# Optimization experiments

Measured on AMD Instinct MI355X. Metric: run time of the kernel, lower is better.

The kernel has to match this reference:

```python
import jax, jax.numpy as jnp
import numpy as np

B, C, H, W = 32, 128, 32, 32
E, K, D, HID = 16, 2, 128, 512  # nbExperts, topK, nbIn=nbOut, hidden=4*max(nbIn,nbOut)


def setup_inputs() -> dict:
    key = jax.random.key(0)
    ks = jax.random.split(key, 6)
    init = lambda k, shape, fan: (jax.random.normal(k, shape, jnp.float32) / np.sqrt(fan)).astype(jnp.float32)
    return {
        "x": jax.random.normal(ks[0], (B, C, H, W), jnp.float32),
        "gate_w": init(ks[1], (D, E), D),
        "gate_b": jnp.zeros((E,), jnp.float32),
        "noise_w": init(ks[2], (D, E), D),
        "noise_b": jnp.zeros((E,), jnp.float32),
        "w1": init(ks[3], (E, D, HID), D),
        "b1": jnp.zeros((E, HID), jnp.float32),
        "w2": init(ks[4], (E, HID, D), HID),
        "b2": jnp.zeros((E, D), jnp.float32),
        "top_k": K,
    }


def reference(x, gate_w, gate_b, noise_w, noise_b, w1, b1, w2, b2, top_k):
    b, c, h, w = x.shape
    xt = x.transpose(0, 2, 3, 1).reshape(-1, c)  # [T, D] tokens (fromCNN path)
    T = xt.shape[0]

    # --- GatingWithNoise: gate(x) + randn * softplus(noise(x)) ---
    logits = xt @ gate_w + gate_b                      # [T, E]
    noise_sd = jax.nn.softplus(xt @ noise_w + noise_b)  # [T, E]
    noise = jax.random.normal(jax.random.key(42), logits.shape, logits.dtype)
    logits = logits + noise * noise_sd

    # --- top-k, softmax over k, scatter to dense [T, E] gate matrix ---
    top_vals, top_idx = jax.lax.top_k(logits, top_k)   # [T, K]
    probs = jax.nn.softmax(top_vals, axis=1)           # [T, K]
    gates = jnp.zeros((T, E), x.dtype).at[jnp.arange(T)[:, None], top_idx].set(probs)

    # --- dense path: run every expert, weighted combine ---
    hdn = jax.nn.relu(jnp.einsum('td,edh->teh', xt, w1) + b1)  # [T, E, HID]
    eo = jnp.einsum('teh,ehd->ted', hdn, w2) + b2              # [T, E, D]
    out = jnp.einsum('te,ted->td', gates, eo)                  # [T, D]

    out = out.reshape(b, h, w, c).transpose(0, 3, 1, 2)        # back to NCHW
    gates = gates.reshape(b, h, w, E)
    return out, gates
```

## Files before the change

### kernel.cpp

```cpp
#include <hip/hip_runtime.h>
#include <stdint.h>

#define NB       32
#define NC       128
#define NHW      1024
#define NT       32768
#define NE       16
#define NHID     512
#define NGBLK    512

typedef __attribute__((ext_vector_type(8))) short short8v;
typedef __attribute__((ext_vector_type(4))) float f32x4;
typedef __attribute__((ext_vector_type(2))) uint32_t uint2v;

__device__ __forceinline__ unsigned short f2bf(float f) {
    uint32_t u = __float_as_uint(f);
    uint32_t r = u + 0x7fffu + ((u >> 16) & 1u);
    return (unsigned short)(r >> 16);
}
__device__ __forceinline__ float bf2f(unsigned short u) {
    return __uint_as_float(((uint32_t)u) << 16);
}

__device__ __forceinline__ void gll16(const void* g, void* l) {
    __builtin_amdgcn_global_load_lds(
        (const __attribute__((address_space(1))) uint32_t*)g,
        (__attribute__((address_space(3))) uint32_t*)l, 16, 0, 0);
}

#define WAIT_VM0_LGKM0() asm volatile("s_waitcnt vmcnt(0) lgkmcnt(0)" ::: "memory")
#define WAIT_LGKM()      asm volatile("s_waitcnt lgkmcnt(0)" ::: "memory")
#define SBAR()           { asm volatile("" ::: "memory"); __builtin_amdgcn_s_barrier(); asm volatile("" ::: "memory"); }

__device__ __forceinline__ uint32_t rotl32(uint32_t x, uint32_t d) {
    return (x << d) | (x >> (32u - d));
}

__device__ __forceinline__ void threefry2x32_20(uint32_t k0, uint32_t k1,
                                                uint32_t& x0, uint32_t& x1) {
    const uint32_t ks0 = k0, ks1 = k1, ks2 = k0 ^ k1 ^ 0x1BD11BDAu;
    x0 += ks0; x1 += ks1;
#define TFR(r) { x0 += x1; x1 = rotl32(x1, r); x1 ^= x0; }
    TFR(13u) TFR(15u) TFR(26u) TFR(6u)
    x0 += ks1; x1 += ks2 + 1u;
    TFR(17u) TFR(29u) TFR(16u) TFR(24u)
    x0 += ks2; x1 += ks0 + 2u;
    TFR(13u) TFR(15u) TFR(26u) TFR(6u)
    x0 += ks0; x1 += ks1 + 3u;
    TFR(17u) TFR(29u) TFR(16u) TFR(24u)
    x0 += ks1; x1 += ks2 + 4u;
    TFR(13u) TFR(15u) TFR(26u) TFR(6u)
    x0 += ks2; x1 += ks0 + 5u;
#undef TFR
}

__device__ __forceinline__ float erfinv_xla_f32(float x) {
    float w = -log1pf(-x * x);
    float p;
    if (w < 5.0f) {
        w = w - 2.5f;
        p = 2.81022636e-08f;
        p = fmaf(p, w, 3.43273939e-07f);
        p = fmaf(p, w, -3.5233877e-06f);
        p = fmaf(p, w, -4.39150654e-06f);
        p = fmaf(p, w, 0.00021858087f);
        p = fmaf(p, w, -0.00125372503f);
        p = fmaf(p, w, -0.00417768164f);
        p = fmaf(p, w, 0.246640727f);
        p = fmaf(p, w, 1.50140941f);
    } else {
        w = sqrtf(w) - 3.0f;
        p = -0.000200214257f;
        p = fmaf(p, w, 0.000100950558f);
        p = fmaf(p, w, 0.00134934322f);
        p = fmaf(p, w, -0.00367342844f);
        p = fmaf(p, w, 0.00573950773f);
        p = fmaf(p, w, -0.0076224613f);
        p = fmaf(p, w, 0.00943887047f);
        p = fmaf(p, w, 1.00167406f);
        p = fmaf(p, w, 2.83297682f);
    }
    return p * x;
}

__device__ __forceinline__ float jax_noise_elem(uint32_t i) {
    uint32_t x0 = 0u, x1 = i;
    threefry2x32_20(0u, 42u, x0, x1);
    uint32_t bits = x0 ^ x1;
    float f = __uint_as_float(0x3f800000u | (bits >> 9)) - 1.0f;
    const float lo = -0.99999994f;
    float u = f * 2.0f + lo;
    u = fmaxf(lo, u);
    return 1.41421354f * erfinv_xla_f32(u);
}

__global__ __launch_bounds__(256) void moe_gate_tw_kernel(
    const float* __restrict__ x,
    const float* __restrict__ gate_w, const float* __restrict__ gate_b,
    const float* __restrict__ noise_w, const float* __restrict__ noise_b,
    float* __restrict__ gates_out,
    int*   __restrict__ top_idx,
    float* __restrict__ top_prob,
    int*   __restrict__ rank,
    int*   __restrict__ bcnt,
    unsigned short* __restrict__ xtb,
    const float* __restrict__ w1, unsigned short* __restrict__ w1bt,
    const float* __restrict__ w2, unsigned short* __restrict__ w2bt,
    int do_new)
{
    __shared__ union { float lw[32 * 160]; float ts[64][65]; } sm;
    __shared__ int lcnt[16];

    const int tid = threadIdx.x;

    if (blockIdx.x >= NGBLK) {
        int blk = blockIdx.x - NGBLK;
        const float* src;  unsigned short* dst;  int R, C;
        if (blk < 256) { src = w1; dst = w1bt; R = 128; C = 512; }
        else           { src = w2; dst = w2bt; R = 512; C = 128; blk -= 256; }
        const int nr = R >> 6, ncc = C >> 6;
        const int e = blk / (nr * ncc);
        const int rem = blk % (nr * ncc);
        const int rt = rem / ncc, ct = rem % ncc;
        const float* S = src + (size_t)e * R * C + (size_t)(rt * 64) * C + ct * 64;
        unsigned short* D = dst + (size_t)e * R * C + (size_t)(ct * 64) * R + rt * 64;
        #pragma unroll
        for (int i = 0; i < 16; ++i) {
            int lin = i * 256 + tid;
            int r = lin >> 6, c = lin & 63;
            sm.ts[r][c] = S[(size_t)r * C + c];
        }
        __syncthreads();
        #pragma unroll
        for (int i = 0; i < 16; ++i) {
            int lin = i * 256 + tid;
            int c = lin >> 6, r = lin & 63;
            D[(size_t)c * R + r] = f2bf(sm.ts[r][c]);
        }
        return;
    }

    const int tl  = tid >> 2;
    const int q   = tid & 3;
    const int t   = blockIdx.x * 64 + tl;
    const int b   = t >> 10, hw = t & 1023;

    if (tid < 16) lcnt[tid] = 0;

    for (int idx = tid; idx < 4096; idx += 256) {
        int ci = idx >> 7;
        int r  = idx & 127;
        int qq = r >> 5, e = r & 31;
        int c  = qq * 32 + ci;
        float v = (e < 16) ? gate_w[c * 16 + e] : noise_w[c * 16 + (e - 16)];
        sm.lw[ci * 160 + qq * 40 + e] = v;
    }
    __syncthreads();

    float acc[32];
    #pragma unroll
    for (int e = 0; e < 32; ++e) acc[e] = 0.f;

    unsigned short xh[32];
    const float* xq = x + (size_t)b * (NC * NHW) + (size_t)(q * 32) * NHW + hw;
    const float* wq = sm.lw + q * 40;
    #pragma unroll 4
    for (int ci = 0; ci < 32; ++ci) {
        float xv = xq[(size_t)ci << 10];
        xh[ci] = f2bf(xv);
        const f32x4* wr = (const f32x4*)(wq + ci * 160);
        #pragma unroll
        for (int j = 0; j < 8; ++j) {
            f32x4 w4 = wr[j];
            #pragma unroll
            for (int k = 0; k < 4; ++k)
                acc[j * 4 + k] = fmaf(xv, w4[k], acc[j * 4 + k]);
        }
    }

    if (do_new) {
        #pragma unroll
        for (int j = 0; j < 4; ++j) {
            short8v v;
            #pragma unroll
            for (int k = 0; k < 8; ++k) v[k] = (short)xh[j * 8 + k];
            *(short8v*)(xtb + (size_t)t * 128 + q * 32 + j * 8) = v;
        }
    }

    #pragma unroll
    for (int e = 0; e < 32; ++e) {
        acc[e] += __shfl_xor(acc[e], 1);
        acc[e] += __shfl_xor(acc[e], 2);
    }

    float lg[4];
    #pragma unroll
    for (int j = 0; j < 4; ++j) {
        int e = q * 4 + j;
        float g  = acc[e] + gate_b[e];
        float an = acc[16 + e] + noise_b[e];
        float sd = fmaxf(an, 0.f) + log1pf(expf(-fabsf(an)));
        float nz = jax_noise_elem((uint32_t)t * 16u + (uint32_t)e);
        lg[j] = fmaf(nz, sd, g);
    }

    float v1 = lg[0], v2 = -INFINITY;
    int   i1 = q * 4, i2 = 0x7fffffff;
    #pragma unroll
    for (int j = 1; j < 4; ++j) {
        float v = lg[j]; int e = q * 4 + j;
        if (v > v1) { v2 = v1; i2 = i1; v1 = v; i1 = e; }
        else if (v > v2) { v2 = v; i2 = e; }
    }
    #pragma unroll
    for (int m = 1; m <= 2; m <<= 1) {
        float pv1 = __shfl_xor(v1, m), pv2 = __shfl_xor(v2, m);
        int   pi1 = __shfl_xor(i1, m), pi2 = __shfl_xor(i2, m);
        bool pBest = (pv1 > v1) || (pv1 == v1 && pi1 < i1);
        float c2v; int c2i;
        if (pBest) { c2v = v1;  c2i = i1;  v1 = pv1; i1 = pi1;
                     if (!((c2v > pv2) || (c2v == pv2 && c2i < pi2))) { c2v = pv2; c2i = pi2; }
        } else     { c2v = pv1; c2i = pi1;
                     if (!((c2v > v2)  || (c2v == v2  && c2i < i2)))  { c2v = v2;  c2i = i2;  }
        }
        v2 = c2v; i2 = c2i;
    }

    float qq = expf(v2 - v1);
    float s  = 1.0f + qq;
    float p1 = 1.0f / s;
    float p2 = qq / s;

    f32x4 g4;
    #pragma unroll
    for (int j = 0; j < 4; ++j) {
        int e = q * 4 + j;
        g4[j] = (e == i1) ? p1 : ((e == i2) ? p2 : 0.f);
    }
    *(f32x4*)(gates_out + (size_t)t * 16 + q * 4) = g4;

    if (q == 0) {
        top_idx[t * 2 + 0] = i1;  top_idx[t * 2 + 1] = i2;
        top_prob[t * 2 + 0] = p1; top_prob[t * 2 + 1] = p2;
        if (do_new) {
            int r1 = atomicAdd(&lcnt[i1], 1);
            int r2 = atomicAdd(&lcnt[i2], 1);
            rank[t * 2 + 0] = r1;
            rank[t * 2 + 1] = r2;
        }
    }
    if (do_new) {
        __syncthreads();
        if (tid < 16) bcnt[blockIdx.x * 16 + tid] = lcnt[tid];
    }
}

__global__ __launch_bounds__(256) void scan_kernel(
    const int* __restrict__ bcnt,
    int* __restrict__ poff, int* __restrict__ blk2e,
    int* __restrict__ blk2chunk, int* __restrict__ total_chunks,
    int* __restrict__ bbase,
    int* __restrict__ pair_tok)
{
    __shared__ int ps[16][17];
    __shared__ int gb[16][17];
    __shared__ int scnt[16];
    __shared__ int snch[16];
    __shared__ int scum[17];
    __shared__ int spoff[16];
    const int tid = threadIdx.x;
    const int e = tid >> 4, g = tid & 15;

    int s = 0;
    for (int b = g * 32; b < g * 32 + 32; ++b)
        s += bcnt[b * 16 + e];
    ps[e][g] = s;
    __syncthreads();

    if (tid < 16) {
        int run = 0;
        for (int gg = 0; gg < 16; ++gg) { gb[tid][gg] = run; run += ps[tid][gg]; }
        scnt[tid] = run;
        snch[tid] = (run + 127) >> 7;
    }
    __syncthreads();

    if (tid == 0) {
        int cc = 0, off = 0;
        for (int ee = 0; ee < 16; ++ee) {
            scum[ee] = cc; spoff[ee] = off;
            cc += snch[ee]; off += snch[ee] << 7;
        }
        scum[16] = cc;
        *total_chunks = cc;
    }
    __syncthreads();
    const int tot = scum[16];
    for (int idx = tid; idx < tot; idx += 256) {
        int ee = 0;
        #pragma unroll
        for (int k = 0; k < 15; ++k)
            if (idx >= scum[k + 1]) ee = k + 1;
        blk2e[idx] = ee;
        blk2chunk[idx] = idx - scum[ee];
    }
    if (tid < 16) poff[tid] = spoff[tid];

    {
        int run = spoff[e] + gb[e][g];
        for (int b = g * 32; b < g * 32 + 32; ++b) {
            bbase[b * 16 + e] = run;
            run += bcnt[b * 16 + e];
        }
    }

    for (int ee = 0; ee < 16; ++ee) {
        int start = spoff[ee] + scnt[ee];
        int end   = spoff[ee] + (snch[ee] << 7);
        for (int i = start + tid; i < end; i += 256)
            pair_tok[i] = -1;
    }
}

__global__ __launch_bounds__(256) void scatter_kernel(
    const int* __restrict__ top_idx, const int* __restrict__ rank,
    const int* __restrict__ bbase, int* __restrict__ pair_tok,
    int* __restrict__ slot_of)
{
    int i = blockIdx.x * 256 + threadIdx.x;
    int t = i >> 1;
    int e = top_idx[i];
    int slot = bbase[(t >> 6) * 16 + e] + rank[i];
    pair_tok[slot] = t;
    slot_of[i] = slot;
}

__device__ __forceinline__ void stage_w1(const unsigned short* w1e, short* W1s,
                                         int hcn, int wid, int lane) {
    #pragma unroll
    for (int k2 = 0; k2 < 2; ++k2) {
        int i2 = wid * 2 + k2;
        int r2 = i2 * 4 + (lane >> 4);
        int s2 = lane & 15;
        gll16(w1e + (size_t)(hcn + r2) * 128 + ((s2 ^ (r2 & 15)) * 8),
              W1s + i2 * 512);
    }
}
__device__ __forceinline__ void stage_w2(const unsigned short* w2e, short* W2s,
                                         int hcn, int wid, int lane) {
    #pragma unroll
    for (int k2 = 0; k2 < 2; ++k2) {
        int i2 = wid * 2 + k2;
        int r2 = i2 * 8 + (lane >> 3);
        int s2 = lane & 7;
        gll16(w2e + (size_t)r2 * 512 + hcn + ((s2 ^ (r2 & 7)) * 8),
              W2s + i2 * 512);
    }
}

__global__ __launch_bounds__(512, 4) void moe_mfma_kernel(
    const unsigned short* __restrict__ xtb,
    const int* __restrict__ pair_tok, const int* __restrict__ blk2e,
    const int* __restrict__ blk2chunk, const int* __restrict__ poff,
    const int* __restrict__ total_chunks,
    const unsigned short* __restrict__ w1bt,
    const float* __restrict__ b1,
    const unsigned short* __restrict__ w2bt,
    const float* __restrict__ b2,
    unsigned short* __restrict__ pair_y)
{
    __shared__ short Hs[128 * 64];
    __shared__ short W1s[64 * 128];
    __shared__ short W2s[128 * 64];

    const int blk = (blockIdx.x & 7) * 66 + (blockIdx.x >> 3);
    if (blk >= *total_chunks) return;
    const int e  = blk2e[blk];
    const int p0 = poff[e] + (blk2chunk[blk] << 7);
    const int tid  = threadIdx.x;
    const int lane = tid & 63;
    const int wid  = tid >> 6;
    const int wm   = wid >> 2;
    const int wn   = wid & 3;
    const int l16  = lane & 15;
    const int lg   = lane >> 4;

    const unsigned short* w1e = w1bt + (size_t)e * 512 * 128;
    const unsigned short* w2e = w2bt + (size_t)e * 128 * 512;

    stage_w1(w1e, W1s, 0, wid, lane);
    stage_w2(w2e, W2s, 0, wid, lane);

    short8v xa[2][4];
    #pragma unroll
    for (int ni = 0; ni < 2; ++ni) {
        int row = wn * 32 + ni * 16 + l16;
        int tok = pair_tok[p0 + row];
        #pragma unroll
        for (int kk = 0; kk < 4; ++kk) {
            short8v v = {};
            if (tok >= 0)
                v = *(const short8v*)(xtb + (size_t)tok * 128 + kk * 32 + lg * 8);
            xa[ni][kk] = v;
        }
    }

    f32x4 yacc[2][4];
    #pragma unroll
    for (int af = 0; af < 2; ++af)
        #pragma unroll
        for (int nj = 0; nj < 4; ++nj)
            yacc[af][nj] = (f32x4){0.f, 0.f, 0.f, 0.f};

    const int rowA0 = wn * 32 + l16, rowA1 = rowA0 + 16;

    for (int c = 0; c < 8; ++c) {
        WAIT_VM0_LGKM0(); SBAR();

        f32x4 hacc[2][2];
        #pragma unroll
        for (int mi = 0; mi < 2; ++mi)
            #pragma unroll
            for (int ni = 0; ni < 2; ++ni)
                hacc[mi][ni] = (f32x4){0.f, 0.f, 0.f, 0.f};

        __builtin_amdgcn_s_setprio(1);
        #pragma unroll
        for (int kk = 0; kk < 4; ++kk) {
            int slot = kk * 4 + lg;
            #pragma unroll
            for (int mi = 0; mi < 2; ++mi) {
                int hr = wm * 32 + mi * 16 + l16;
                short8v wfr = *(const short8v*)(W1s + hr * 128 + ((slot ^ (hr & 15)) * 8));
                #pragma unroll
                for (int ni = 0; ni < 2; ++ni)
                    hacc[mi][ni] = __builtin_amdgcn_mfma_f32_16x16x32_bf16(
                        wfr, xa[ni][kk], hacc[mi][ni], 0, 0, 0);
            }
        }
        __builtin_amdgcn_s_setprio(0);

        #pragma unroll
        for (int mi = 0; mi < 2; ++mi) {
            int h0 = wm * 32 + mi * 16 + lg * 4;
            f32x4 b1v = *(const f32x4*)(b1 + e * 512 + (c << 6) + h0);
            #pragma unroll
            for (int ni = 0; ni < 2; ++ni) {
                int tok = wn * 32 + ni * 16 + l16;
                float v0 = fmaxf(hacc[mi][ni][0] + b1v[0], 0.f);
                float v1 = fmaxf(hacc[mi][ni][1] + b1v[1], 0.f);
                float v2 = fmaxf(hacc[mi][ni][2] + b1v[2], 0.f);
                float v3 = fmaxf(hacc[mi][ni][3] + b1v[3], 0.f);
                uint32_t lo = (uint32_t)f2bf(v0) | ((uint32_t)f2bf(v1) << 16);
                uint32_t hi = (uint32_t)f2bf(v2) | ((uint32_t)f2bf(v3) << 16);
                int slot = h0 >> 3;
                int addr = tok * 64 + ((slot ^ (tok & 7)) << 3) + (h0 & 7);
                *(uint2v*)(Hs + addr) = (uint2v){lo, hi};
            }
        }
        WAIT_LGKM(); SBAR();

        if (c < 7) stage_w1(w1e, W1s, (c + 1) << 6, wid, lane);

        __builtin_amdgcn_s_setprio(1);
        #pragma unroll
        for (int kk = 0; kk < 2; ++kk) {
            int slot = kk * 4 + lg;
            short8v a0 = *(const short8v*)(Hs + rowA0 * 64 + ((slot ^ (rowA0 & 7)) * 8));
            short8v a1 = *(const short8v*)(Hs + rowA1 * 64 + ((slot ^ (rowA1 & 7)) * 8));
            #pragma unroll
            for (int nj = 0; nj < 4; ++nj) {
                int dr = wm * 64 + nj * 16 + l16;
                short8v bfr = *(const short8v*)(W2s + dr * 64 + ((slot ^ (dr & 7)) * 8));
                yacc[0][nj] = __builtin_amdgcn_mfma_f32_16x16x32_bf16(a0, bfr, yacc[0][nj], 0, 0, 0);
                yacc[1][nj] = __builtin_amdgcn_mfma_f32_16x16x32_bf16(a1, bfr, yacc[1][nj], 0, 0, 0);
            }
        }
        __builtin_amdgcn_s_setprio(0);
        WAIT_LGKM(); SBAR();

        if (c < 7) stage_w2(w2e, W2s, (c + 1) << 6, wid, lane);
    }

    #pragma unroll
    for (int nj = 0; nj < 4; ++nj) {
        int d = wm * 64 + nj * 16 + l16;
        float b2v = b2[e * 128 + d];
        #pragma unroll
        for (int af = 0; af < 2; ++af) {
            #pragma unroll
            for (int r = 0; r < 4; ++r) {
                int m = wn * 32 + af * 16 + lg * 4 + r;
                pair_y[(size_t)(p0 + m) * 128 + d] = f2bf(yacc[af][nj][r] + b2v);
            }
        }
    }
}

__global__ __launch_bounds__(256) void combine_kernel(
    const unsigned short* __restrict__ pair_y, const int* __restrict__ slot_of,
    const float* __restrict__ top_prob, float* __restrict__ out)
{
    __shared__ float ob[64][129];
    const int blk = blockIdx.x;
    const int b = blk >> 4;
    const int hw0 = (blk & 15) << 6;
    const int tid = threadIdx.x;
    #pragma unroll
    for (int i = 0; i < 4; ++i) {
        int lin = i * 256 + tid;
        int tl = lin >> 4, dg = lin & 15;
        int t = b * 1024 + hw0 + tl;
        int s0 = slot_of[t * 2], s1 = slot_of[t * 2 + 1];
        float p0 = top_prob[t * 2], p1 = top_prob[t * 2 + 1];
        short8v y0 = *(const short8v*)(pair_y + (size_t)s0 * 128 + dg * 8);
        short8v y1 = *(const short8v*)(pair_y + (size_t)s1 * 128 + dg * 8);
        #pragma unroll
        for (int j = 0; j < 8; ++j)
            ob[tl][dg * 8 + j] = p0 * bf2f((unsigned short)y0[j]) + p1 * bf2f((unsigned short)y1[j]);
    }
    __syncthreads();
    #pragma unroll
    for (int i = 0; i < 32; ++i) {
        int lin = i * 256 + tid;
        int d = lin >> 6, hwl = lin & 63;
        out[((size_t)b * 128 + d) * 1024 + hw0 + hwl] = ob[hwl][d];
    }
}

__global__ __launch_bounds__(256) void moe_expert_kernel(
    const float* __restrict__ x,
    const int* __restrict__ top_idx, const float* __restrict__ top_prob,
    const float* __restrict__ w1, const float* __restrict__ b1,
    const float* __restrict__ w2, const float* __restrict__ b2,
    float* __restrict__ out)
{
    __shared__ float xsB[128];
    __shared__ float hb[512];

    const int tid = threadIdx.x;
    const int t = blockIdx.x;
    const int b = t >> 10, hw = t & 1023;

    if (tid < 128)
        xsB[tid] = x[((size_t)b * 128 + tid) * NHW + hw];
    __syncthreads();

    float oacc = 0.f;
    #pragma unroll
    for (int k = 0; k < 2; ++k) {
        const int e = top_idx[t * 2 + k];
        const float pw = top_prob[t * 2 + k];
        const float* W1 = w1 + (size_t)e * (128 * 512);
        float a0 = 0.f, a1 = 0.f;
        for (int d = 0; d < 128; ++d) {
            float xv = xsB[d];
            a0 = fmaf(xv, W1[d * 512 + tid], a0);
            a1 = fmaf(xv, W1[d * 512 + tid + 256], a1);
        }
        hb[tid]       = fmaxf(a0 + b1[e * 512 + tid], 0.f);
        hb[tid + 256] = fmaxf(a1 + b1[e * 512 + tid + 256], 0.f);
        __syncthreads();
        if (tid < 128) {
            const float* W2 = w2 + (size_t)e * (512 * 128);
            float a = 0.f;
            for (int h = 0; h < 512; ++h)
                a = fmaf(hb[h], W2[h * 128 + tid], a);
            oacc = fmaf(pw, a + b2[e * 128 + tid], oacc);
        }
        __syncthreads();
    }
    if (tid < 128)
        out[((size_t)b * 128 + tid) * NHW + hw] = oacc;
}

extern "C" void kernel_launch(void* const* d_in, const int* in_sizes, int n_in,
                              void* d_out, int out_size, void* d_ws, size_t ws_size,
                              hipStream_t stream) {
    const float* x       = (const float*)d_in[0];
    const float* gate_w  = (const float*)d_in[1];
    const float* gate_b  = (const float*)d_in[2];
    const float* noise_w = (const float*)d_in[3];
    const float* noise_b = (const float*)d_in[4];
    const float* w1      = (const float*)d_in[5];
    const float* b1      = (const float*)d_in[6];
    const float* w2      = (const float*)d_in[7];
    const float* b2      = (const float*)d_in[8];

    float* out   = (float*)d_out;
    float* gates = out + (size_t)NB * NC * NHW;

    const size_t OFF_POFF   = 0;
    const size_t OFF_TOTAL  = 1024;
    const size_t OFF_B2E    = 4096;
    const size_t OFF_B2C    = 8192;
    const size_t OFF_TIDX   = 12288;
    const size_t OFF_RANK   = OFF_TIDX  + (size_t)NT * 2 * 4;
    const size_t OFF_SLOT   = OFF_RANK  + (size_t)NT * 2 * 4;
    const size_t OFF_PROB   = OFF_SLOT  + (size_t)NT * 2 * 4;
    const size_t OFF_BCNT   = OFF_PROB  + (size_t)NT * 2 * 4;
    const size_t OFF_BBASE  = OFF_BCNT  + (size_t)NGBLK * 16 * 4;
    const size_t OFF_XTB    = OFF_BBASE + (size_t)NGBLK * 16 * 4;
    const size_t OFF_W1BT   = OFF_XTB   + (size_t)NT * 128 * 2;
    const size_t OFF_W2BT   = OFF_W1BT  + (size_t)NE * 512 * 128 * 2;
    const size_t OFF_PTOK   = OFF_W2BT  + (size_t)NE * 128 * 512 * 2;
    const size_t NPAIR_PAD  = 67584;
    const size_t OFF_PAIRY  = OFF_PTOK  + NPAIR_PAD * 4;
    const size_t NEED       = OFF_PAIRY + NPAIR_PAD * 128 * 2;

    char* ws = (char*)d_ws;
    int*   poff     = (int*)(ws + OFF_POFF);
    int*   total_ch = (int*)(ws + OFF_TOTAL);
    int*   blk2e    = (int*)(ws + OFF_B2E);
    int*   blk2c    = (int*)(ws + OFF_B2C);
    int*   top_idx  = (int*)(ws + OFF_TIDX);
    int*   rank     = (int*)(ws + OFF_RANK);
    int*   slot_of  = (int*)(ws + OFF_SLOT);
    float* top_prob = (float*)(ws + OFF_PROB);
    int*   bcnt     = (int*)(ws + OFF_BCNT);
    int*   bbase    = (int*)(ws + OFF_BBASE);
    unsigned short* xtb    = (unsigned short*)(ws + OFF_XTB);
    unsigned short* w1bt   = (unsigned short*)(ws + OFF_W1BT);
    unsigned short* w2bt   = (unsigned short*)(ws + OFF_W2BT);
    int*   pair_tok = (int*)(ws + OFF_PTOK);
    unsigned short* pair_y = (unsigned short*)(ws + OFF_PAIRY);

    const int use_new = (ws_size >= NEED) ? 1 : 0;

    moe_gate_tw_kernel<<<use_new ? (NGBLK + 512) : NGBLK, 256, 0, stream>>>(
        x, gate_w, gate_b, noise_w, noise_b,
        gates, top_idx, top_prob, rank, bcnt, xtb,
        w1, w1bt, w2, w2bt, use_new);

    if (use_new) {
        scan_kernel<<<1, 256, 0, stream>>>(bcnt, poff, blk2e, blk2c, total_ch,
                                           bbase, pair_tok);
        scatter_kernel<<<NT * 2 / 256, 256, 0, stream>>>(top_idx, rank, bbase,
                                                         pair_tok, slot_of);
        moe_mfma_kernel<<<528, 512, 0, stream>>>(
            xtb, pair_tok, blk2e, blk2c, poff, total_ch,
            w1bt, b1, w2bt, b2, pair_y);
        combine_kernel<<<512, 256, 0, stream>>>(pair_y, slot_of, top_prob, out);
    } else {
        moe_expert_kernel<<<NT, 256, 0, stream>>>(
            x, top_idx, top_prob, w1, b1, w2, b2, out);
    }
}
```

Before: 94.09 us.

## Load expert weights directly from global into registers, double-buffer hidden LDS tile

```diff
diff --git a/kernel.cpp b/kernel.cpp
--- a/kernel.cpp
+++ b/kernel.cpp
@@ -22,13 +22,6 @@
     return __uint_as_float(((uint32_t)u) << 16);
 }
 
-__device__ __forceinline__ void gll16(const void* g, void* l) {
-    __builtin_amdgcn_global_load_lds(
-        (const __attribute__((address_space(1))) uint32_t*)g,
-        (__attribute__((address_space(3))) uint32_t*)l, 16, 0, 0);
-}
-
-#define WAIT_VM0_LGKM0() asm volatile("s_waitcnt vmcnt(0) lgkmcnt(0)" ::: "memory")
 #define WAIT_LGKM()      asm volatile("s_waitcnt lgkmcnt(0)" ::: "memory")
 #define SBAR()           { asm volatile("" ::: "memory"); __builtin_amdgcn_s_barrier(); asm volatile("" ::: "memory"); }
 
@@ -336,30 +329,7 @@
     slot_of[i] = slot;
 }
 
-__device__ __forceinline__ void stage_w1(const unsigned short* w1e, short* W1s,
-                                         int hcn, int wid, int lane) {
-    #pragma unroll
-    for (int k2 = 0; k2 < 2; ++k2) {
-        int i2 = wid * 2 + k2;
-        int r2 = i2 * 4 + (lane >> 4);
-        int s2 = lane & 15;
-        gll16(w1e + (size_t)(hcn + r2) * 128 + ((s2 ^ (r2 & 15)) * 8),
-              W1s + i2 * 512);
-    }
-}
-__device__ __forceinline__ void stage_w2(const unsigned short* w2e, short* W2s,
-                                         int hcn, int wid, int lane) {
-    #pragma unroll
-    for (int k2 = 0; k2 < 2; ++k2) {
-        int i2 = wid * 2 + k2;
-        int r2 = i2 * 8 + (lane >> 3);
-        int s2 = lane & 7;
-        gll16(w2e + (size_t)r2 * 512 + hcn + ((s2 ^ (r2 & 7)) * 8),
-              W2s + i2 * 512);
-    }
-}
-
-__global__ __launch_bounds__(512, 4) void moe_mfma_kernel(
+__global__ __launch_bounds__(512, 3) void moe_mfma_kernel(
     const unsigned short* __restrict__ xtb,
     const int* __restrict__ pair_tok, const int* __restrict__ blk2e,
     const int* __restrict__ blk2chunk, const int* __restrict__ poff,
@@ -370,9 +340,7 @@
     const float* __restrict__ b2,
     unsigned short* __restrict__ pair_y)
 {
-    __shared__ short Hs[128 * 64];
-    __shared__ short W1s[64 * 128];
-    __shared__ short W2s[128 * 64];
+    __shared__ short Hs[2][128 * 64];
 
     const int blk = (blockIdx.x & 7) * 66 + (blockIdx.x >> 3);
     if (blk >= *total_chunks) return;
@@ -389,9 +357,6 @@
     const unsigned short* w1e = w1bt + (size_t)e * 512 * 128;
     const unsigned short* w2e = w2bt + (size_t)e * 128 * 512;
 
-    stage_w1(w1e, W1s, 0, wid, lane);
-    stage_w2(w2e, W2s, 0, wid, lane);
-
     short8v xa[2][4];
     #pragma unroll
     for (int ni = 0; ni < 2; ++ni) {
@@ -416,7 +381,7 @@
     const int rowA0 = wn * 32 + l16, rowA1 = rowA0 + 16;
 
     for (int c = 0; c < 8; ++c) {
-        WAIT_VM0_LGKM0(); SBAR();
+        short* Hb = (short*)Hs[c & 1];
 
         f32x4 hacc[2][2];
         #pragma unroll
@@ -431,8 +396,8 @@
             int slot = kk * 4 + lg;
             #pragma unroll
             for (int mi = 0; mi < 2; ++mi) {
-                int hr = wm * 32 + mi * 16 + l16;
-                short8v wfr = *(const short8v*)(W1s + hr * 128 + ((slot ^ (hr & 15)) * 8));
+                int hr = (c << 6) + wm * 32 + mi * 16 + l16;
+                short8v wfr = *(const short8v*)(w1e + (size_t)hr * 128 + slot * 8);
                 #pragma unroll
                 for (int ni = 0; ni < 2; ++ni)
                     hacc[mi][ni] = __builtin_amdgcn_mfma_f32_16x16x32_bf16(
@@ -455,32 +420,27 @@
                 uint32_t lo = (uint32_t)f2bf(v0) | ((uint32_t)f2bf(v1) << 16);
                 uint32_t hi = (uint32_t)f2bf(v2) | ((uint32_t)f2bf(v3) << 16);
                 int slot = h0 >> 3;
-                int addr = tok * 64 + ((slot ^ (tok & 7)) << 3) + (h0 & 7);
-                *(uint2v*)(Hs + addr) = (uint2v){lo, hi};
+                int addr = tok * 64 + (((slot ^ (tok & 7))) << 3) + (h0 & 7);
+                *(uint2v*)(Hb + addr) = (uint2v){lo, hi};
             }
         }
         WAIT_LGKM(); SBAR();
-
-        if (c < 7) stage_w1(w1e, W1s, (c + 1) << 6, wid, lane);
 
         __builtin_amdgcn_s_setprio(1);
         #pragma unroll
         for (int kk = 0; kk < 2; ++kk) {
             int slot = kk * 4 + lg;
-            short8v a0 = *(const short8v*)(Hs + rowA0 * 64 + ((slot ^ (rowA0 & 7)) * 8));
-            short8v a1 = *(const short8v*)(Hs + rowA1 * 64 + ((slot ^ (rowA1 & 7)) * 8));
+            short8v a0 = *(const short8v*)(Hb + rowA0 * 64 + ((slot ^ (rowA0 & 7)) * 8));
+            short8v a1 = *(const short8v*)(Hb + rowA1 * 64 + ((slot ^ (rowA1 & 7)) * 8));
             #pragma unroll
             for (int nj = 0; nj < 4; ++nj) {
                 int dr = wm * 64 + nj * 16 + l16;
-                short8v bfr = *(const short8v*)(W2s + dr * 64 + ((slot ^ (dr & 7)) * 8));
+                short8v bfr = *(const short8v*)(w2e + (size_t)dr * 512 + (c << 6) + slot * 8);
                 yacc[0][nj] = __builtin_amdgcn_mfma_f32_16x16x32_bf16(a0, bfr, yacc[0][nj], 0, 0, 0);
                 yacc[1][nj] = __builtin_amdgcn_mfma_f32_16x16x32_bf16(a1, bfr, yacc[1][nj], 0, 0, 0);
             }
         }
         __builtin_amdgcn_s_setprio(0);
-        WAIT_LGKM(); SBAR();
-
-        if (c < 7) stage_w2(w2e, W2s, (c + 1) << 6, wid, lane);
     }
 
     #pragma unroll
```

After: 159.6 us. 1.7x slower.

## Fuse scan into scatter kernel and relax vmcnt wait in MFMA loop

Applied to the files above, without the earlier changes.

```diff
diff --git a/kernel.cpp b/kernel.cpp
--- a/kernel.cpp
+++ b/kernel.cpp
@@ -28,6 +28,7 @@
         (__attribute__((address_space(3))) uint32_t*)l, 16, 0, 0);
 }
 
+#define WAIT_VM2_LGKM0() asm volatile("s_waitcnt vmcnt(2) lgkmcnt(0)" ::: "memory")
 #define WAIT_VM0_LGKM0() asm volatile("s_waitcnt vmcnt(0) lgkmcnt(0)" ::: "memory")
 #define WAIT_LGKM()      asm volatile("s_waitcnt lgkmcnt(0)" ::: "memory")
 #define SBAR()           { asm volatile("" ::: "memory"); __builtin_amdgcn_s_barrier(); asm volatile("" ::: "memory"); }
@@ -256,31 +257,33 @@
     }
 }
 
-__global__ __launch_bounds__(256) void scan_kernel(
+__global__ __launch_bounds__(256) void scatter2_kernel(
     const int* __restrict__ bcnt,
+    const int* __restrict__ top_idx, const int* __restrict__ rank,
     int* __restrict__ poff, int* __restrict__ blk2e,
     int* __restrict__ blk2chunk, int* __restrict__ total_chunks,
-    int* __restrict__ bbase,
-    int* __restrict__ pair_tok)
+    int* __restrict__ pair_tok, int* __restrict__ slot_of)
 {
     __shared__ int ps[16][17];
-    __shared__ int gb[16][17];
+    __shared__ int cum[16][17];
     __shared__ int scnt[16];
     __shared__ int snch[16];
     __shared__ int scum[17];
     __shared__ int spoff[16];
+    __shared__ int lbase[2][16];
+
     const int tid = threadIdx.x;
-    const int e = tid >> 4, g = tid & 15;
-
-    int s = 0;
-    for (int b = g * 32; b < g * 32 + 32; ++b)
-        s += bcnt[b * 16 + e];
-    ps[e][g] = s;
+    const int e = tid >> 4, s = tid & 15;
+
+    int a = 0;
+    for (int b = s * 32; b < s * 32 + 32; ++b)
+        a += bcnt[b * 16 + e];
+    ps[e][s] = a;
     __syncthreads();
 
     if (tid < 16) {
         int run = 0;
-        for (int gg = 0; gg < 16; ++gg) { gb[tid][gg] = run; run += ps[tid][gg]; }
+        for (int ss = 0; ss < 16; ++ss) { cum[tid][ss] = run; run += ps[tid][ss]; }
         scnt[tid] = run;
         snch[tid] = (run + 127) >> 7;
     }
@@ -293,45 +296,44 @@
             cc += snch[ee]; off += snch[ee] << 7;
         }
         scum[16] = cc;
-        *total_chunks = cc;
     }
     __syncthreads();
-    const int tot = scum[16];
-    for (int idx = tid; idx < tot; idx += 256) {
-        int ee = 0;
-        #pragma unroll
-        for (int k = 0; k < 15; ++k)
-            if (idx >= scum[k + 1]) ee = k + 1;
-        blk2e[idx] = ee;
-        blk2chunk[idx] = idx - scum[ee];
-    }
-    if (tid < 16) poff[tid] = spoff[tid];
-
-    {
-        int run = spoff[e] + gb[e][g];
-        for (int b = g * 32; b < g * 32 + 32; ++b) {
-            bbase[b * 16 + e] = run;
-            run += bcnt[b * 16 + e];
-        }
-    }
-
-    for (int ee = 0; ee < 16; ++ee) {
-        int start = spoff[ee] + scnt[ee];
-        int end   = spoff[ee] + (snch[ee] << 7);
-        for (int i = start + tid; i < end; i += 256)
-            pair_tok[i] = -1;
-    }
-}
-
-__global__ __launch_bounds__(256) void scatter_kernel(
-    const int* __restrict__ top_idx, const int* __restrict__ rank,
-    const int* __restrict__ bbase, int* __restrict__ pair_tok,
-    int* __restrict__ slot_of)
-{
-    int i = blockIdx.x * 256 + threadIdx.x;
+
+    if (tid < 32) {
+        int ee = tid >> 1, w = tid & 1;
+        int g = (int)blockIdx.x * 2 + w;
+        int sg = g >> 5;
+        int part = cum[ee][sg];
+        for (int b = sg * 32; b < g; ++b) part += bcnt[b * 16 + ee];
+        lbase[w][ee] = spoff[ee] + part;
+    }
+
+    if (blockIdx.x == 0) {
+        if (tid < 16) poff[tid] = spoff[tid];
+        if (tid == 0) *total_chunks = scum[16];
+        const int tot = scum[16];
+        for (int idx = tid; idx < tot; idx += 256) {
+            int ee = 0;
+            #pragma unroll
+            for (int k = 0; k < 15; ++k)
+                if (idx >= scum[k + 1]) ee = k + 1;
+            blk2e[idx] = ee;
+            blk2chunk[idx] = idx - scum[ee];
+        }
+        for (int ee = 0; ee < 16; ++ee) {
+            int start = spoff[ee] + scnt[ee];
+            int end   = spoff[ee] + (snch[ee] << 7);
+            for (int i = start + tid; i < end; i += 256)
+                pair_tok[i] = -1;
+        }
+    }
+    __syncthreads();
+
+    int i = (int)blockIdx.x * 256 + tid;
     int t = i >> 1;
-    int e = top_idx[i];
-    int slot = bbase[(t >> 6) * 16 + e] + rank[i];
+    int ee = top_idx[i];
+    int g = (t >> 6) & 1;
+    int slot = lbase[g][ee] + rank[i];
     pair_tok[slot] = t;
     slot_of[i] = slot;
 }
@@ -416,7 +418,7 @@
     const int rowA0 = wn * 32 + l16, rowA1 = rowA0 + 16;
 
     for (int c = 0; c < 8; ++c) {
-        WAIT_VM0_LGKM0(); SBAR();
+        WAIT_VM2_LGKM0(); SBAR();
 
         f32x4 hacc[2][2];
         #pragma unroll
@@ -459,7 +461,7 @@
                 *(uint2v*)(Hs + addr) = (uint2v){lo, hi};
             }
         }
-        WAIT_LGKM(); SBAR();
+        WAIT_VM0_LGKM0(); SBAR();
 
         if (c < 7) stage_w1(w1e, W1s, (c + 1) << 6, wid, lane);
 
@@ -600,8 +602,7 @@
     const size_t OFF_SLOT   = OFF_RANK  + (size_t)NT * 2 * 4;
     const size_t OFF_PROB   = OFF_SLOT  + (size_t)NT * 2 * 4;
     const size_t OFF_BCNT   = OFF_PROB  + (size_t)NT * 2 * 4;
-    const size_t OFF_BBASE  = OFF_BCNT  + (size_t)NGBLK * 16 * 4;
-    const size_t OFF_XTB    = OFF_BBASE + (size_t)NGBLK * 16 * 4;
+    const size_t OFF_XTB    = OFF_BCNT  + (size_t)NGBLK * 16 * 4;
     const size_t OFF_W1BT   = OFF_XTB   + (size_t)NT * 128 * 2;
     const size_t OFF_W2BT   = OFF_W1BT  + (size_t)NE * 512 * 128 * 2;
     const size_t OFF_PTOK   = OFF_W2BT  + (size_t)NE * 128 * 512 * 2;
@@ -619,7 +620,6 @@
     int*   slot_of  = (int*)(ws + OFF_SLOT);
     float* top_prob = (float*)(ws + OFF_PROB);
     int*   bcnt     = (int*)(ws + OFF_BCNT);
-    int*   bbase    = (int*)(ws + OFF_BBASE);
     unsigned short* xtb    = (unsigned short*)(ws + OFF_XTB);
     unsigned short* w1bt   = (unsigned short*)(ws + OFF_W1BT);
     unsigned short* w2bt   = (unsigned short*)(ws + OFF_W2BT);
@@ -634,10 +634,9 @@
         w1, w1bt, w2, w2bt, use_new);
 
     if (use_new) {
-        scan_kernel<<<1, 256, 0, stream>>>(bcnt, poff, blk2e, blk2c, total_ch,
-                                           bbase, pair_tok);
-        scatter_kernel<<<NT * 2 / 256, 256, 0, stream>>>(top_idx, rank, bbase,
-                                                         pair_tok, slot_of);
+        scatter2_kernel<<<256, 256, 0, stream>>>(bcnt, top_idx, rank,
+                                                 poff, blk2e, blk2c, total_ch,
+                                                 pair_tok, slot_of);
         moe_mfma_kernel<<<528, 512, 0, stream>>>(
             xtb, pair_tok, blk2e, blk2c, poff, total_ch,
             w1bt, b1, w2bt, b2, pair_y);
```

Measured after the change: 87.27 us (median of 2 runs). -7.3%, faster.
